# Kernel optimization log

Measured on AMD Instinct MI355X. Metric: run time of the kernel, lower is better.

Reference implementation:

```python
import jax, jax.numpy as jnp
import numpy as np

H = 16          # num_heads
LN_EPS = 1e-5   # torch LayerNorm default


def _ln(x, g, b):
    m = jnp.mean(x, axis=-1, keepdims=True)
    v = jnp.var(x, axis=-1, keepdims=True)
    return (x - m) * jax.lax.rsqrt(v + LN_EPS) * g + b


def _cross_attn(xq, xkv, wq, wk, wv, wp, bp):
    B, N, C = xq.shape
    d = C // H
    scale = d ** -0.5
    q = (xq @ wq).reshape(B, N, H, d).transpose(0, 2, 1, 3)   # bhnd
    k = (xkv @ wk).reshape(B, N, H, d).transpose(0, 2, 1, 3)
    v = (xkv @ wv).reshape(B, N, H, d).transpose(0, 2, 1, 3)
    attn = jax.nn.softmax(jnp.einsum('bhnd,bhmd->bhnm', q, k) * scale, axis=-1)
    out = jnp.einsum('bhnm,bhmd->bhnd', attn, v).transpose(0, 2, 1, 3).reshape(B, N, C)
    return out @ wp + bp


def setup_inputs() -> dict:
    key = jax.random.key(0)
    ks = jax.random.split(key, 16)
    B, N, C, Hid = 8, 1024, 1024, 4096
    s = 0.02
    inp = {
        'x_1': jax.random.normal(ks[0], (B, N, C), jnp.float32),
        'x_2': jax.random.normal(ks[1], (B, N, C), jnp.float32),
        'x_3': jax.random.normal(ks[2], (B, N, C), jnp.float32),
        'ln11_g': jnp.ones((C,), jnp.float32), 'ln11_b': jnp.zeros((C,), jnp.float32),
        'ln12_g': jnp.ones((C,), jnp.float32), 'ln12_b': jnp.zeros((C,), jnp.float32),
        'ln21_g': jnp.ones((C,), jnp.float32), 'ln21_b': jnp.zeros((C,), jnp.float32),
        'ln23_g': jnp.ones((C,), jnp.float32), 'ln23_b': jnp.zeros((C,), jnp.float32),
        'ln2_g': jnp.ones((C,), jnp.float32), 'ln2_b': jnp.zeros((C,), jnp.float32),
        'a1_wq': s * jax.random.normal(ks[3], (C, C), jnp.float32),
        'a1_wk': s * jax.random.normal(ks[4], (C, C), jnp.float32),
        'a1_wv': s * jax.random.normal(ks[5], (C, C), jnp.float32),
        'a1_wp': s * jax.random.normal(ks[6], (C, C), jnp.float32),
        'a1_bp': jnp.zeros((C,), jnp.float32),
        'a2_wq': s * jax.random.normal(ks[7], (C, C), jnp.float32),
        'a2_wk': s * jax.random.normal(ks[8], (C, C), jnp.float32),
        'a2_wv': s * jax.random.normal(ks[9], (C, C), jnp.float32),
        'a2_wp': s * jax.random.normal(ks[10], (C, C), jnp.float32),
        'a2_bp': jnp.zeros((C,), jnp.float32),
        'fc1_w': s * jax.random.normal(ks[11], (C, Hid), jnp.float32),
        'fc1_b': jnp.zeros((Hid,), jnp.float32),
        'fc2_w': s * jax.random.normal(ks[12], (Hid, C), jnp.float32),
        'fc2_b': jnp.zeros((C,), jnp.float32),
    }
    return inp


def reference(x_1, x_2, x_3,
              ln11_g, ln11_b, ln12_g, ln12_b, ln21_g, ln21_b, ln23_g, ln23_b,
              ln2_g, ln2_b,
              a1_wq, a1_wk, a1_wv, a1_wp, a1_bp,
              a2_wq, a2_wk, a2_wv, a2_wp, a2_bp,
              fc1_w, fc1_b, fc2_w, fc2_b):
    # dual cross-attention branches + residual (drop_path/dropout are identity at p=0)
    br1 = _cross_attn(_ln(x_1, ln11_g, ln11_b), _ln(x_2, ln12_g, ln12_b),
                      a1_wq, a1_wk, a1_wv, a1_wp, a1_bp)
    br2 = _cross_attn(_ln(x_1, ln21_g, ln21_b), _ln(x_3, ln23_g, ln23_b),
                      a2_wq, a2_wk, a2_wv, a2_wp, a2_bp)
    x = x_1 + br1 + br2
    # MLP block
    h = jax.nn.gelu(_ln(x, ln2_g, ln2_b) @ fc1_w + fc1_b, approximate=False)
    x = x + (h @ fc2_w + fc2_b)
    return x
```

## Files before the change

kernel.cpp:

```cpp
#include <hip/hip_runtime.h>
#include <hip/hip_bf16.h>
#include <cstdint>

typedef unsigned short u16;
typedef __bf16 v8bf __attribute__((ext_vector_type(8)));
typedef short v4s __attribute__((ext_vector_type(4)));
typedef float v4f __attribute__((ext_vector_type(4)));

__device__ __forceinline__ u16 f2bf(float f) {
  union { float f; uint32_t u; } v; v.f = f;
  return (u16)((v.u + 0x7fffu + ((v.u >> 16) & 1u)) >> 16);
}
__device__ __forceinline__ float bf2f(u16 u) {
  union { uint32_t u; float f; } v; v.u = ((uint32_t)u) << 16; return v.f;
}

#define GLL16(gsrc, ldst) \
  __builtin_amdgcn_global_load_lds((__attribute__((address_space(1))) void*)(gsrc), \
      (__attribute__((address_space(3))) void*)(ldst), 16, 0, 0)

#define TILE_MAP(blk, bm, bn) \
  int bm = ((blk) & 7) * 8 + (((blk) >> 3) & 7); \
  int bn = (blk) >> 6;

__device__ __forceinline__ void gemm_core(
    const u16* __restrict__ A, const u16* __restrict__ Bt, int K,
    char* la, char* lb, int bm, int bn, int tid, v4f acc[4][4])
{
  int wv = tid >> 6, lane = tid & 63, quad = lane >> 4, lc = lane & 15;
  int wm = wv & 1, wn = wv >> 1;
  for (int kt = 0; kt < K; kt += 64) {
    __syncthreads();
    #pragma unroll
    for (int c0 = 0; c0 < 4; ++c0) {
      int chunk = wv*4 + c0;
      int off = chunk*1024 + lane*16;
      int row = off >> 7;
      int sc  = (off >> 4) & 7;
      int lg  = sc ^ (row & 7);
      GLL16(A  + (size_t)(bm*128 + row) * K + kt + lg*8, la + chunk*1024);
      GLL16(Bt + (size_t)(bn*128 + row) * K + kt + lg*8, lb + chunk*1024);
    }
    __syncthreads();
    #pragma unroll
    for (int kc = 0; kc < 2; ++kc) {
      v8bf af[4], bfr[4];
      #pragma unroll
      for (int r = 0; r < 4; ++r) {
        int row = wm*64 + r*16 + lc;
        int sc = (kc*4 + quad) ^ (row & 7);
        af[r] = *(const v8bf*)(la + row*128 + sc*16);
      }
      #pragma unroll
      for (int c = 0; c < 4; ++c) {
        int row = wn*64 + c*16 + lc;
        int sc = (kc*4 + quad) ^ (row & 7);
        bfr[c] = *(const v8bf*)(lb + row*128 + sc*16);
      }
      #pragma unroll
      for (int r = 0; r < 4; ++r)
        #pragma unroll
        for (int c = 0; c < 4; ++c)
          acc[r][c] = __builtin_amdgcn_mfma_f32_16x16x32_bf16(af[r], bfr[c], acc[r][c], 0, 0, 0);
    }
  }
}

template<int NT>
__device__ __forceinline__ void gemm8_core(
    const u16* __restrict__ A, const u16* __restrict__ Bt,
    char* lds, int bm, int bn, int tid, v4f acc[8][4])
{
  constexpr int K = NT * 64;
  int wid = tid >> 6, lane = tid & 63, quad = lane >> 4, lc = lane & 15;
  int wm = wid >> 2, wn = wid & 3;

  int ch0 = wid*2, ch1 = wid*2 + 1;
  int r0 = ch0*8 + (lane >> 3), r1 = ch1*8 + (lane >> 3);
  int lg0 = (lane & 7) ^ (r0 & 7), lg1 = (lane & 7) ^ (r1 & 7);
  const u16* gA0 = A  + (size_t)(bm*256 + r0) * K + lg0*8;
  const u16* gA1 = A  + (size_t)(bm*256 + r1) * K + lg1*8;
  const u16* gB0 = Bt + (size_t)(bn*256 + r0) * K + lg0*8;
  const u16* gB1 = Bt + (size_t)(bn*256 + r1) * K + lg1*8;
  int dA0 = ch0*1024, dA1 = ch1*1024;

  auto STAGE_A = [&](int h, int tile, int buf) {
    GLL16(gA0 + (size_t)h*128*K + tile*64, lds + buf*32768 + h*16384 + dA0);
    GLL16(gA1 + (size_t)h*128*K + tile*64, lds + buf*32768 + h*16384 + dA1);
  };
  auto STAGE_B = [&](int h, int tile, int buf) {
    GLL16(gB0 + (size_t)h*128*K + tile*64, lds + 65536 + buf*32768 + h*16384 + dA0);
    GLL16(gB1 + (size_t)h*128*K + tile*64, lds + 65536 + buf*32768 + h*16384 + dA1);
  };

  int s0 = quad ^ (lc & 7);
  const char* rA0 = lds + ((wm*128 + lc)*128 + s0*16);
  const char* rA1 = lds + ((wm*128 + lc)*128 + (s0^4)*16);
  const char* rB0 = lds + 65536 + ((wn*64 + lc)*128 + s0*16);
  const char* rB1 = lds + 65536 + ((wn*64 + lc)*128 + (s0^4)*16);

  v8bf a[4][2], b0[2][2], b1[2][2];

#define RD_A(qm) do { _Pragma("unroll") for (int mf = 0; mf < 4; ++mf) { \
    a[mf][0] = *(const v8bf*)(rA0 + bsel*32768 + (qm)*8192 + mf*2048); \
    a[mf][1] = *(const v8bf*)(rA1 + bsel*32768 + (qm)*8192 + mf*2048); } } while(0)
#define RD_B(qn, bb) do { _Pragma("unroll") for (int nf = 0; nf < 2; ++nf) { \
    bb[nf][0] = *(const v8bf*)(rB0 + bsel*32768 + (qn)*4096 + nf*2048); \
    bb[nf][1] = *(const v8bf*)(rB1 + bsel*32768 + (qn)*4096 + nf*2048); } } while(0)
#define MFMAQ(qm, bb, qn) do { \
    __builtin_amdgcn_s_setprio(1); \
    _Pragma("unroll") for (int mf = 0; mf < 4; ++mf) \
    _Pragma("unroll") for (int nf = 0; nf < 2; ++nf) \
    _Pragma("unroll") for (int kc = 0; kc < 2; ++kc) \
      acc[(qm)*4+mf][(qn)*2+nf] = __builtin_amdgcn_mfma_f32_16x16x32_bf16( \
          a[mf][kc], bb[nf][kc], acc[(qm)*4+mf][(qn)*2+nf], 0, 0, 0); \
    __builtin_amdgcn_s_setprio(0); } while(0)
#define LGKM0 do { asm volatile("s_waitcnt lgkmcnt(0)" ::: "memory"); \
    __builtin_amdgcn_sched_barrier(0); } while(0)

#define GROUP(t, bs) do { \
    const int bsel = (bs); const int nsel = bsel ^ 1; \
     \
    RD_A(0); RD_B(0, b0); \
    if ((t)+1 < NT) STAGE_A(0, (t)+1, nsel); \
    __builtin_amdgcn_s_barrier(); LGKM0; \
    MFMAQ(0, b0, 0); \
    __builtin_amdgcn_s_barrier(); \
     \
    RD_B(1, b1); \
    if ((t)+1 < NT) STAGE_A(1, (t)+1, nsel); \
    __builtin_amdgcn_s_barrier(); LGKM0; \
    MFMAQ(0, b1, 1); \
    __builtin_amdgcn_s_barrier(); \
     \
    RD_A(1); \
    if ((t)+2 < NT) STAGE_B(0, (t)+2, bsel); \
    __builtin_amdgcn_s_barrier(); LGKM0; \
    MFMAQ(1, b1, 1); \
    __builtin_amdgcn_s_barrier(); \
     \
    if ((t)+2 < NT) STAGE_B(1, (t)+2, bsel); \
    __builtin_amdgcn_s_barrier(); \
    MFMAQ(1, b0, 0); \
    if ((t) < NT-2)       asm volatile("s_waitcnt vmcnt(4)" ::: "memory"); \
    else if ((t) == NT-2) asm volatile("s_waitcnt vmcnt(0)" ::: "memory"); \
    __builtin_amdgcn_s_barrier(); \
  } while(0)

  STAGE_B(0, 0, 0); STAGE_B(1, 0, 0);
  STAGE_A(0, 0, 0); STAGE_A(1, 0, 0);
  STAGE_B(0, 1, 1); STAGE_B(1, 1, 1);
  asm volatile("s_waitcnt vmcnt(4)" ::: "memory");
  __builtin_amdgcn_s_barrier();

  #pragma unroll 1
  for (int ti = 0; ti < NT; ti += 2) {
    GROUP(ti, 0);
    GROUP(ti + 1, 1);
  }

#undef RD_A
#undef RD_B
#undef MFMAQ
#undef LGKM0
#undef GROUP
}

struct TDesc { const float* W; u16* WT; int K, N, tstart; };
struct PrepArgs {
  TDesc d[10];
  const float* lx[4]; const float* lg[4]; const float* lb_[4]; u16* lo[4];
  int ts;
};
__global__ __launch_bounds__(256) void prep_kernel(PrepArgs P)
{
  __shared__ float sh[32*33];
  int tid = threadIdx.x;
  if ((int)blockIdx.x < P.ts) {
    int bi = blockIdx.x;
    int idx = 0;
    #pragma unroll
    for (int i = 1; i < 10; ++i) if (bi >= P.d[i].tstart) idx = i;
    const float* W = P.d[idx].W;
    u16* WT = P.d[idx].WT;
    int K = P.d[idx].K, N = P.d[idx].N;
    int loc = bi - P.d[idx].tstart;
    int tiles_n = N >> 5;
    int bn = loc % tiles_n, bk = loc / tiles_n;
    int tx = tid & 31, ty = tid >> 5;
    #pragma unroll
    for (int j = 0; j < 4; ++j)
      sh[(ty + j*8)*33 + tx] = W[(size_t)(bk*32 + ty + j*8) * N + bn*32 + tx];
    __syncthreads();
    #pragma unroll
    for (int j = 0; j < 4; ++j)
      WT[(size_t)(bn*32 + ty + j*8) * K + bk*32 + tx] = f2bf(sh[tx*33 + ty + j*8]);
  } else {
    int lid = blockIdx.x - P.ts;
    int id = lid >> 13, row = lid & 8191;
    const float4* xr = (const float4*)(P.lx[id] + (size_t)row * 1024);
    float4 v = xr[tid];
    float s = v.x + v.y + v.z + v.w;
    float ss = v.x*v.x + v.y*v.y + v.z*v.z + v.w*v.w;
    for (int d = 1; d < 64; d <<= 1) { s += __shfl_xor(s, d); ss += __shfl_xor(ss, d); }
    int wv = tid >> 6, lane = tid & 63;
    if (lane == 0) { sh[wv] = s; sh[4 + wv] = ss; }
    __syncthreads();
    s  = sh[0] + sh[1] + sh[2] + sh[3];
    ss = sh[4] + sh[5] + sh[6] + sh[7];
    float mean = s * (1.f/1024.f);
    float var  = ss * (1.f/1024.f) - mean*mean;
    float rs = rsqrtf(var + 1e-5f);
    float4 gv = ((const float4*)P.lg[id])[tid];
    float4 bv = ((const float4*)P.lb_[id])[tid];
    ushort4 o;
    o.x = f2bf((v.x-mean)*rs*gv.x + bv.x);
    o.y = f2bf((v.y-mean)*rs*gv.y + bv.y);
    o.z = f2bf((v.z-mean)*rs*gv.z + bv.z);
    o.w = f2bf((v.w-mean)*rs*gv.w + bv.w);
    ((ushort4*)P.lo[id])[(size_t)row*256 + tid] = o;
  }
}

__global__ __launch_bounds__(256) void ln_bf16_kernel(
    const u16* __restrict__ x, const float* __restrict__ g, const float* __restrict__ bt,
    u16* __restrict__ out)
{
  int row = blockIdx.x, tid = threadIdx.x;
  ushort4 xr = ((const ushort4*)x)[(size_t)row*256 + tid];
  float4 v;
  v.x = bf2f(xr.x); v.y = bf2f(xr.y); v.z = bf2f(xr.z); v.w = bf2f(xr.w);
  float s = v.x + v.y + v.z + v.w;
  float ss = v.x*v.x + v.y*v.y + v.z*v.z + v.w*v.w;
  for (int d = 1; d < 64; d <<= 1) { s += __shfl_xor(s, d); ss += __shfl_xor(ss, d); }
  __shared__ float red[8];
  int wv = tid >> 6, lane = tid & 63;
  if (lane == 0) { red[wv] = s; red[4 + wv] = ss; }
  __syncthreads();
  s  = red[0] + red[1] + red[2] + red[3];
  ss = red[4] + red[5] + red[6] + red[7];
  float mean = s * (1.f/1024.f);
  float var  = ss * (1.f/1024.f) - mean*mean;
  float rs = rsqrtf(var + 1e-5f);
  float4 gv = ((const float4*)g)[tid];
  float4 bv = ((const float4*)bt)[tid];
  ushort4 o;
  o.x = f2bf((v.x-mean)*rs*gv.x + bv.x);
  o.y = f2bf((v.y-mean)*rs*gv.y + bv.y);
  o.z = f2bf((v.z-mean)*rs*gv.z + bv.z);
  o.w = f2bf((v.w-mean)*rs*gv.w + bv.w);
  ((ushort4*)out)[(size_t)row*256 + tid] = o;
}

struct QkvArgs { const u16* A[3]; const u16* Bt[3]; u16* C[3]; };
__global__ __launch_bounds__(512, 2) void gemm8_qkv(QkvArgs P)
{
  __shared__ __align__(16) char lds8[131072];
  int sub = blockIdx.x >> 7;
  int local = blockIdx.x & 127;
  int bm = (local & 7)*4 + ((local >> 3) & 3), bn = local >> 5;
  v4f acc[8][4] = {};
  gemm8_core<16>(P.A[sub], P.Bt[sub], lds8, bm, bn, threadIdx.x, acc);

  int tid = threadIdx.x, wid = tid >> 6, lane = tid & 63, quad = lane >> 4, lc = lane & 15;
  int wm = wid >> 2, wn = wid & 3;
  u16* Cout = P.C[sub];
  #pragma unroll
  for (int mf = 0; mf < 8; ++mf) {
    int grow = bm*256 + wm*128 + mf*16 + quad*4;
    #pragma unroll
    for (int nf = 0; nf < 4; ++nf) {
      int gcol = bn*256 + wn*64 + nf*16 + lc;
      if (sub == 2) {
        ushort4 o;
        o.x = f2bf(acc[mf][nf][0]); o.y = f2bf(acc[mf][nf][1]);
        o.z = f2bf(acc[mf][nf][2]); o.w = f2bf(acc[mf][nf][3]);
        *(ushort4*)(Cout + (size_t)gcol * 8192 + grow) = o;
      } else {
        #pragma unroll
        for (int i = 0; i < 4; ++i)
          Cout[(size_t)(grow + i) * 1024 + gcol] = f2bf(acc[mf][nf][i]);
      }
    }
  }
}

__device__ __forceinline__ void attn_body(
    const u16* __restrict__ Q, const u16* __restrict__ K, const u16* __restrict__ VT,
    u16* __restrict__ O, int bid, int tid, char* lds_)
{
  int qt = bid & 15, h = (bid >> 4) & 15, b = bid >> 8;
  int wv = tid >> 6, lane = tid & 63, quad = lane >> 4, lc = lane & 15;
  char* kt_l = lds_;
  char* vt_l = lds_ + 16384;
  const float scale = 0.125f;

  v8bf qf[2];
  {
    int qrow = qt*64 + wv*16 + lc;
    const u16* qp = Q + ((size_t)(b*1024 + qrow) * 1024 + h*64 + quad*8);
    qf[0] = *(const v8bf*)qp;
    qf[1] = *(const v8bf*)(qp + 32);
  }

  float m_i = -1e30f, l_i = 0.f;
  v4f oacc[4] = {};

  for (int it = 0; it < 8; ++it) {
    int kvb = it * 128;
    __syncthreads();
    #pragma unroll
    for (int c0 = 0; c0 < 4; ++c0) {
      int ch = wv*4 + c0;
      int off = ch*1024 + lane*16;
      {
        int row = off >> 7, sc = (off >> 4) & 7, lg = sc ^ (row & 7);
        GLL16(K + (size_t)(b*1024 + kvb + row) * 1024 + h*64 + lg*8, kt_l + ch*1024);
      }
      {
        int row = off >> 8, sc = (off >> 4) & 15, lg = sc ^ (row & 15);
        GLL16(VT + (size_t)(h*64 + row) * 8192 + b*1024 + kvb + lg*8, vt_l + ch*1024);
      }
    }
    __syncthreads();

    v4f s[8] = {};
    #pragma unroll
    for (int ct = 0; ct < 8; ++ct) {
      int row = ct*16 + lc;
      #pragma unroll
      for (int kc = 0; kc < 2; ++kc) {
        int sc = (kc*4 + quad) ^ (row & 7);
        v8bf kf = *(const v8bf*)(kt_l + row*128 + sc*16);
        s[ct] = __builtin_amdgcn_mfma_f32_16x16x32_bf16(kf, qf[kc], s[ct], 0, 0, 0);
      }
    }

    float mx = m_i;
    #pragma unroll
    for (int ct = 0; ct < 8; ++ct)
      #pragma unroll
      for (int i = 0; i < 4; ++i) mx = fmaxf(mx, s[ct][i] * scale);
    mx = fmaxf(mx, __shfl_xor(mx, 16));
    mx = fmaxf(mx, __shfl_xor(mx, 32));
    float alpha = __expf(m_i - mx);
    float rs = 0.f;
    #pragma unroll
    for (int ct = 0; ct < 8; ++ct)
      #pragma unroll
      for (int i = 0; i < 4; ++i) {
        float p = __expf(s[ct][i] * scale - mx);
        s[ct][i] = p;
        rs += p;
      }
    rs += __shfl_xor(rs, 16);
    rs += __shfl_xor(rs, 32);
    l_i = l_i * alpha + rs;
    m_i = mx;
    #pragma unroll
    for (int dt = 0; dt < 4; ++dt)
      #pragma unroll
      for (int i = 0; i < 4; ++i) oacc[dt][i] *= alpha;

    #pragma unroll
    for (int ct = 0; ct < 8; ++ct) {
      v4s pfrag;
      #pragma unroll
      for (int i = 0; i < 4; ++i) pfrag[i] = (short)f2bf(s[ct][i]);
      int lg = ct*2 + (quad >> 1);
      int ho = (quad & 1) * 8;
      #pragma unroll
      for (int dt = 0; dt < 4; ++dt) {
        int rowd = dt*16 + lc;
        int sc = lg ^ (rowd & 15);
        v4s vfrag = *(const v4s*)(vt_l + rowd*256 + sc*16 + ho);
        oacc[dt] = __builtin_amdgcn_mfma_f32_16x16x16bf16_1k(vfrag, pfrag, oacc[dt], 0, 0, 0);
      }
    }
  }

  __syncthreads();
  {
    char* base = kt_l + wv*2048;
    float inv = 1.f / l_i;
    #pragma unroll
    for (int dt = 0; dt < 4; ++dt) {
      ushort4 o;
      o.x = f2bf(oacc[dt][0]*inv); o.y = f2bf(oacc[dt][1]*inv);
      o.z = f2bf(oacc[dt][2]*inv); o.w = f2bf(oacc[dt][3]*inv);
      int lg = dt*2 + (quad >> 1);
      int sc = lg ^ (lc & 7);
      *(ushort4*)(base + lc*128 + sc*16 + (quad & 1)*8) = o;
    }
  }
  __syncthreads();
  {
    char* base = kt_l + wv*2048;
    #pragma unroll
    for (int rep = 0; rep < 2; ++rep) {
      int qr = rep*8 + (lane >> 3);
      int ch = lane & 7;
      int sc = ch ^ (qr & 7);
      uint4 d = *(const uint4*)(base + qr*128 + sc*16);
      *(uint4*)(O + (size_t)(b*1024 + qt*64 + wv*16 + qr) * 1024 + h*64 + ch*8) = d;
    }
  }
}

__global__ __launch_bounds__(256, 4) void attn_kernel(
    const u16* __restrict__ Q, const u16* __restrict__ K, const u16* __restrict__ VT,
    u16* __restrict__ O)
{
  __shared__ __align__(16) char lds_[32768];
  attn_body(Q, K, VT, O, blockIdx.x, threadIdx.x, lds_);
}

__global__ __launch_bounds__(256, 3) void attn_proj_kernel(
    const u16* __restrict__ Q, const u16* __restrict__ K, const u16* __restrict__ VT,
    u16* __restrict__ O,
    const u16* __restrict__ GA, const u16* __restrict__ GBt,
    const float* __restrict__ Gbias, u16* __restrict__ GC)
{
  __shared__ __align__(16) char lds_[32768];
  int tid = threadIdx.x;
  if ((int)blockIdx.x < 2048) {
    attn_body(Q, K, VT, O, blockIdx.x, tid, lds_);
  } else {
    int local = blockIdx.x - 2048;
    TILE_MAP(local, bm, bn)
    int wv = tid >> 6, lane = tid & 63, quad = lane >> 4, lc = lane & 15;
    int wm = wv & 1, wn = wv >> 1;
    v4f acc[4][4] = {};
    gemm_core(GA, GBt, 1024, lds_, lds_ + 16384, bm, bn, tid, acc);
    #pragma unroll
    for (int r = 0; r < 4; ++r) {
      int grow = bm*128 + wm*64 + r*16 + quad*4;
      #pragma unroll
      for (int c = 0; c < 4; ++c) {
        int gcol = bn*128 + wn*64 + c*16 + lc;
        float bv = Gbias[gcol];
        #pragma unroll
        for (int i = 0; i < 4; ++i)
          GC[(size_t)(grow + i) * 1024 + gcol] = f2bf(acc[r][c][i] + bv);
      }
    }
  }
}

__global__ __launch_bounds__(256, 3) void gemm_projadd(
    const u16* __restrict__ A, const u16* __restrict__ Bt,
    const float* __restrict__ bias, const float* __restrict__ x1,
    const u16* __restrict__ o1b, u16* __restrict__ xsum)
{
  TILE_MAP((int)blockIdx.x, bm, bn)
  int tid = threadIdx.x, wv = tid >> 6, lane = tid & 63, quad = lane >> 4, lc = lane & 15;
  int wm = wv & 1, wn = wv >> 1;
  __shared__ __align__(16) char lds_[32768];
  v4f acc[4][4] = {};
  gemm_core(A, Bt, 1024, lds_, lds_ + 16384, bm, bn, tid, acc);
  #pragma unroll
  for (int r = 0; r < 4; ++r) {
    int grow = bm*128 + wm*64 + r*16 + quad*4;
    #pragma unroll
    for (int c = 0; c < 4; ++c) {
      int gcol = bn*128 + wn*64 + c*16 + lc;
      float bv = bias[gcol];
      #pragma unroll
      for (int i = 0; i < 4; ++i) {
        size_t idx = (size_t)(grow + i) * 1024 + gcol;
        xsum[idx] = f2bf(acc[r][c][i] + bv + x1[idx] + bf2f(o1b[idx]));
      }
    }
  }
}

__global__ __launch_bounds__(512, 2) void gemm_fc1(
    const u16* __restrict__ A, const u16* __restrict__ Bt,
    const float* __restrict__ bias, u16* __restrict__ C)
{
  __shared__ __align__(16) char lds8[131072];
  int blk = blockIdx.x;
  int bm = (blk & 7)*4 + ((blk >> 3) & 3), bn = blk >> 5;
  v4f acc[8][4] = {};
  gemm8_core<16>(A, Bt, lds8, bm, bn, threadIdx.x, acc);

  int tid = threadIdx.x, wid = tid >> 6, lane = tid & 63, quad = lane >> 4, lc = lane & 15;
  int wm = wid >> 2, wn = wid & 3;
  #pragma unroll
  for (int nf = 0; nf < 4; ++nf) {
    int gcol = bn*256 + wn*64 + nf*16 + lc;
    float bv = bias[gcol];
    #pragma unroll
    for (int mf = 0; mf < 8; ++mf) {
      int grow = bm*256 + wm*128 + mf*16 + quad*4;
      #pragma unroll
      for (int i = 0; i < 4; ++i) {
        float v = acc[mf][nf][i] + bv;
        float u2 = fminf(1.5957691216f * (v + 0.044715f * v * v * v), 80.f);
        float t = __expf(u2);
        float ge = v * t / (t + 1.f);
        C[(size_t)(grow + i) * 4096 + gcol] = f2bf(ge);
      }
    }
  }
}

__global__ __launch_bounds__(256, 3) void gemm_fc2(
    const u16* __restrict__ A, const u16* __restrict__ Bt,
    const float* __restrict__ bias, const u16* __restrict__ r1,
    float* __restrict__ C)
{
  TILE_MAP((int)blockIdx.x, bm, bn)
  int tid = threadIdx.x, wv = tid >> 6, lane = tid & 63, quad = lane >> 4, lc = lane & 15;
  int wm = wv & 1, wn = wv >> 1;
  __shared__ __align__(16) char lds_[32768];
  v4f acc[4][4] = {};
  gemm_core(A, Bt, 4096, lds_, lds_ + 16384, bm, bn, tid, acc);
  #pragma unroll
  for (int r = 0; r < 4; ++r) {
    int grow = bm*128 + wm*64 + r*16 + quad*4;
    #pragma unroll
    for (int c = 0; c < 4; ++c) {
      int gcol = bn*128 + wn*64 + c*16 + lc;
      float bv = bias[gcol];
      #pragma unroll
      for (int i = 0; i < 4; ++i) {
        size_t idx = (size_t)(grow + i) * 1024 + gcol;
        C[idx] = acc[r][c][i] + bv + bf2f(r1[idx]);
      }
    }
  }
}

extern "C" void kernel_launch(void* const* d_in, const int* in_sizes, int n_in,
                              void* d_out, int out_size, void* d_ws, size_t ws_size,
                              hipStream_t stream)
{
  const float* x1    = (const float*)d_in[0];
  const float* x2    = (const float*)d_in[1];
  const float* x3    = (const float*)d_in[2];
  const float* ln11g = (const float*)d_in[3];
  const float* ln11b = (const float*)d_in[4];
  const float* ln12g = (const float*)d_in[5];
  const float* ln12b = (const float*)d_in[6];
  const float* ln21g = (const float*)d_in[7];
  const float* ln21b = (const float*)d_in[8];
  const float* ln23g = (const float*)d_in[9];
  const float* ln23b = (const float*)d_in[10];
  const float* ln2g  = (const float*)d_in[11];
  const float* ln2b  = (const float*)d_in[12];
  const float* a1wq  = (const float*)d_in[13];
  const float* a1wk  = (const float*)d_in[14];
  const float* a1wv  = (const float*)d_in[15];
  const float* a1wp  = (const float*)d_in[16];
  const float* a1bp  = (const float*)d_in[17];
  const float* a2wq  = (const float*)d_in[18];
  const float* a2wk  = (const float*)d_in[19];
  const float* a2wv  = (const float*)d_in[20];
  const float* a2wp  = (const float*)d_in[21];
  const float* a2bp  = (const float*)d_in[22];
  const float* fc1w  = (const float*)d_in[23];
  const float* fc1b  = (const float*)d_in[24];
  const float* fc2w  = (const float*)d_in[25];
  const float* fc2b  = (const float*)d_in[26];

  char* ws = (char*)d_ws;
  const size_t MB = (size_t)1 << 20;
  u16* wtq1 = (u16*)(ws + 0*MB);  u16* wtk1 = (u16*)(ws + 2*MB);
  u16* wtv1 = (u16*)(ws + 4*MB);  u16* wtp1 = (u16*)(ws + 6*MB);
  u16* wtq2 = (u16*)(ws + 8*MB);  u16* wtk2 = (u16*)(ws + 10*MB);
  u16* wtv2 = (u16*)(ws + 12*MB); u16* wtp2 = (u16*)(ws + 14*MB);
  u16* wtf1 = (u16*)(ws + 16*MB); u16* wtf2 = (u16*)(ws + 24*MB);
  u16* xq1  = (u16*)(ws + 32*MB); u16* xkv1 = (u16*)(ws + 48*MB);
  u16* xq2  = (u16*)(ws + 64*MB); u16* xkv2 = (u16*)(ws + 80*MB);
  u16* Qb   = (u16*)(ws + 96*MB); u16* Kb   = (u16*)(ws + 112*MB);
  u16* VTb  = (u16*)(ws + 128*MB);
  u16* O1   = (u16*)(ws + 32*MB);
  u16* O2   = (u16*)(ws + 48*MB);
  u16* o1b  = (u16*)(ws + 64*MB);
  u16* xsum = (u16*)(ws + 112*MB);
  u16* ln2o = (u16*)(ws + 32*MB);
  u16* hbuf = (u16*)(ws + 48*MB);

  dim3 blk(256);
  dim3 blk8(512);

  PrepArgs pa;
  const float* Ws[10]  = {a1wq, a1wk, a1wv, a1wp, a2wq, a2wk, a2wv, a2wp, fc1w, fc2w};
  u16* WTs[10]         = {wtq1, wtk1, wtv1, wtp1, wtq2, wtk2, wtv2, wtp2, wtf1, wtf2};
  int Kd[10] = {1024,1024,1024,1024,1024,1024,1024,1024,1024,4096};
  int Nd[10] = {1024,1024,1024,1024,1024,1024,1024,1024,4096,1024};
  int ts = 0;
  for (int i = 0; i < 10; ++i) {
    pa.d[i] = {Ws[i], WTs[i], Kd[i], Nd[i], ts};
    ts += (Kd[i]/32) * (Nd[i]/32);
  }
  pa.ts = ts;
  pa.lx[0]=x1; pa.lg[0]=ln11g; pa.lb_[0]=ln11b; pa.lo[0]=xq1;
  pa.lx[1]=x2; pa.lg[1]=ln12g; pa.lb_[1]=ln12b; pa.lo[1]=xkv1;
  pa.lx[2]=x1; pa.lg[2]=ln21g; pa.lb_[2]=ln21b; pa.lo[2]=xq2;
  pa.lx[3]=x3; pa.lg[3]=ln23g; pa.lb_[3]=ln23b; pa.lo[3]=xkv2;
  prep_kernel<<<ts + 32768, blk, 0, stream>>>(pa);

  QkvArgs g1;
  g1.A[0]=xq1;  g1.Bt[0]=wtq1; g1.C[0]=Qb;
  g1.A[1]=xkv1; g1.Bt[1]=wtk1; g1.C[1]=Kb;
  g1.A[2]=xkv1; g1.Bt[2]=wtv1; g1.C[2]=VTb;
  gemm8_qkv<<<384, blk8, 0, stream>>>(g1);

  attn_kernel<<<2048, blk, 0, stream>>>(Qb, Kb, VTb, O1);

  QkvArgs g2;
  g2.A[0]=xq2;  g2.Bt[0]=wtq2; g2.C[0]=Qb;
  g2.A[1]=xkv2; g2.Bt[1]=wtk2; g2.C[1]=Kb;
  g2.A[2]=xkv2; g2.Bt[2]=wtv2; g2.C[2]=VTb;
  gemm8_qkv<<<384, blk8, 0, stream>>>(g2);

  attn_proj_kernel<<<2048 + 512, blk, 0, stream>>>(Qb, Kb, VTb, O2, O1, wtp1, a1bp, o1b);

  gemm_projadd<<<512, blk, 0, stream>>>(O2, wtp2, a2bp, x1, o1b, xsum);

  ln_bf16_kernel<<<8192, blk, 0, stream>>>(xsum, ln2g, ln2b, ln2o);

  gemm_fc1<<<512, blk8, 0, stream>>>(ln2o, wtf1, fc1b, hbuf);

  gemm_fc2<<<512, blk, 0, stream>>>(hbuf, wtf2, fc2b, xsum, (float*)d_out);
}
```

Measured before the change: 709.1 us.

## Deepen A-tile prefetch in 256x256 GEMM and stage epilogue stores through LDS

The main loop of the 8-wave GEMM core now prefetches A tiles two iterations ahead, as it already did for B, rather than one. All staging is grouped into two points per iteration, one barrier is removed and the vmcnt wait is raised to allow more loads in flight. The QKV (non-transposed outputs) and fc1 epilogues now write bf16 results into LDS and then emit coalesced 16-byte row stores, replacing scattered 2-byte global stores. This trades extra LDS traffic and a block-wide sync for better global write coalescing. The deeper prefetch relies on exact vmcnt accounting and on the double-buffered LDS slots not being overwritten while still being read.

```diff
diff --git a/kernel.cpp b/kernel.cpp
--- a/kernel.cpp
+++ b/kernel.cpp
@@ -119,38 +119,36 @@
     __builtin_amdgcn_sched_barrier(0); } while(0)
 
 #define GROUP(t, bs) do { \
-    const int bsel = (bs); const int nsel = bsel ^ 1; \
+    const int bsel = (bs); \
      \
     RD_A(0); RD_B(0, b0); \
-    if ((t)+1 < NT) STAGE_A(0, (t)+1, nsel); \
     __builtin_amdgcn_s_barrier(); LGKM0; \
     MFMAQ(0, b0, 0); \
     __builtin_amdgcn_s_barrier(); \
      \
     RD_B(1, b1); \
-    if ((t)+1 < NT) STAGE_A(1, (t)+1, nsel); \
     __builtin_amdgcn_s_barrier(); LGKM0; \
     MFMAQ(0, b1, 1); \
     __builtin_amdgcn_s_barrier(); \
      \
     RD_A(1); \
-    if ((t)+2 < NT) STAGE_B(0, (t)+2, bsel); \
+    if ((t)+2 < NT) { STAGE_B(0, (t)+2, bsel); STAGE_B(1, (t)+2, bsel); } \
     __builtin_amdgcn_s_barrier(); LGKM0; \
     MFMAQ(1, b1, 1); \
     __builtin_amdgcn_s_barrier(); \
      \
-    if ((t)+2 < NT) STAGE_B(1, (t)+2, bsel); \
-    __builtin_amdgcn_s_barrier(); \
+    if ((t)+2 < NT) { STAGE_A(0, (t)+2, bsel); STAGE_A(1, (t)+2, bsel); } \
     MFMAQ(1, b0, 0); \
-    if ((t) < NT-2)       asm volatile("s_waitcnt vmcnt(4)" ::: "memory"); \
-    else if ((t) == NT-2) asm volatile("s_waitcnt vmcnt(0)" ::: "memory"); \
+    if ((t)+2 < NT)       asm volatile("s_waitcnt vmcnt(8)" ::: "memory"); \
+    else if ((t)+2 == NT) asm volatile("s_waitcnt vmcnt(0)" ::: "memory"); \
     __builtin_amdgcn_s_barrier(); \
   } while(0)
 
   STAGE_B(0, 0, 0); STAGE_B(1, 0, 0);
   STAGE_A(0, 0, 0); STAGE_A(1, 0, 0);
   STAGE_B(0, 1, 1); STAGE_B(1, 1, 1);
-  asm volatile("s_waitcnt vmcnt(4)" ::: "memory");
+  STAGE_A(0, 1, 1); STAGE_A(1, 1, 1);
+  asm volatile("s_waitcnt vmcnt(8)" ::: "memory");
   __builtin_amdgcn_s_barrier();
 
   #pragma unroll 1
@@ -265,22 +263,38 @@
   int tid = threadIdx.x, wid = tid >> 6, lane = tid & 63, quad = lane >> 4, lc = lane & 15;
   int wm = wid >> 2, wn = wid & 3;
   u16* Cout = P.C[sub];
-  #pragma unroll
-  for (int mf = 0; mf < 8; ++mf) {
-    int grow = bm*256 + wm*128 + mf*16 + quad*4;
-    #pragma unroll
-    for (int nf = 0; nf < 4; ++nf) {
-      int gcol = bn*256 + wn*64 + nf*16 + lc;
-      if (sub == 2) {
+  if (sub == 2) {
+    #pragma unroll
+    for (int mf = 0; mf < 8; ++mf) {
+      int grow = bm*256 + wm*128 + mf*16 + quad*4;
+      #pragma unroll
+      for (int nf = 0; nf < 4; ++nf) {
+        int gcol = bn*256 + wn*64 + nf*16 + lc;
         ushort4 o;
         o.x = f2bf(acc[mf][nf][0]); o.y = f2bf(acc[mf][nf][1]);
         o.z = f2bf(acc[mf][nf][2]); o.w = f2bf(acc[mf][nf][3]);
         *(ushort4*)(Cout + (size_t)gcol * 8192 + grow) = o;
-      } else {
+      }
+    }
+  } else {
+    #pragma unroll
+    for (int mf = 0; mf < 8; ++mf) {
+      int lrow = wm*128 + mf*16 + quad*4;
+      #pragma unroll
+      for (int nf = 0; nf < 4; ++nf) {
+        int lcol = wn*64 + nf*16 + lc;
         #pragma unroll
         for (int i = 0; i < 4; ++i)
-          Cout[(size_t)(grow + i) * 1024 + gcol] = f2bf(acc[mf][nf][i]);
-      }
+          *(u16*)(lds8 + (size_t)(lrow + i)*512 + (size_t)lcol*2) = f2bf(acc[mf][nf][i]);
+      }
+    }
+    __syncthreads();
+    int rr = tid >> 5, cseg = tid & 31;
+    #pragma unroll
+    for (int p = 0; p < 16; ++p) {
+      int row = p*16 + rr;
+      uint4 d = *(const uint4*)(lds8 + (size_t)row*512 + cseg*16);
+      *(uint4*)(Cout + (size_t)(bm*256 + row)*1024 + bn*256 + cseg*8) = d;
     }
   }
 }
@@ -488,20 +502,27 @@
   int wm = wid >> 2, wn = wid & 3;
   #pragma unroll
   for (int nf = 0; nf < 4; ++nf) {
-    int gcol = bn*256 + wn*64 + nf*16 + lc;
-    float bv = bias[gcol];
+    int lcol = wn*64 + nf*16 + lc;
+    float bv = bias[bn*256 + lcol];
     #pragma unroll
     for (int mf = 0; mf < 8; ++mf) {
-      int grow = bm*256 + wm*128 + mf*16 + quad*4;
+      int lrow = wm*128 + mf*16 + quad*4;
       #pragma unroll
       for (int i = 0; i < 4; ++i) {
         float v = acc[mf][nf][i] + bv;
         float u2 = fminf(1.5957691216f * (v + 0.044715f * v * v * v), 80.f);
         float t = __expf(u2);
-        float ge = v * t / (t + 1.f);
-        C[(size_t)(grow + i) * 4096 + gcol] = f2bf(ge);
-      }
-    }
+        *(u16*)(lds8 + (size_t)(lrow + i)*512 + (size_t)lcol*2) = f2bf(v * t / (t + 1.f));
+      }
+    }
+  }
+  __syncthreads();
+  int rr = tid >> 5, cseg = tid & 31;
+  #pragma unroll
+  for (int p = 0; p < 16; ++p) {
+    int row = p*16 + rr;
+    uint4 d = *(const uint4*)(lds8 + (size_t)row*512 + cseg*16);
+    *(uint4*)(C + (size_t)(bm*256 + row)*4096 + bn*256 + cseg*8) = d;
   }
 }
 
```

Result: no change. 712.8 us (+0.5%).
